# Performance work log

Measured on AMD Instinct MI355X. Metric: run time of the kernel, lower is better.

## Reference

```python
import jax, jax.numpy as jnp
import numpy as np

EPS = 1e-8  # torch F.cosine_similarity eps


def _cosine_logits(emb, mem):
    # emb: [N, C], mem: [S, C] -> [N, S]
    num = emb @ mem.T
    denom = jnp.linalg.norm(emb, axis=1, keepdims=True) * jnp.linalg.norm(mem, axis=1)[None, :]
    return num / jnp.maximum(denom, EPS)


def setup_inputs() -> dict:
    key = jax.random.key(0)
    k1, k2, k3, k4 = jax.random.split(key, 4)
    N, S, C = 8192, 4096, 256
    return {
        "face": jax.random.normal(k1, (N, C), dtype=jnp.float32),
        "speech": jax.random.normal(k2, (N, C), dtype=jnp.float32),
        # init.normal_(mean=0, std=0.5)
        "speech_value_memory": 0.5 * jax.random.normal(k3, (S, C), dtype=jnp.float32),
        "face_key_memory": 0.5 * jax.random.normal(k4, (S, C), dtype=jnp.float32),
    }


def reference(face, speech, speech_value_memory, face_key_memory):
    # speech_encoder runs under torch.no_grad() -> stop_gradient; encoders abstracted as identity.
    speech_emb = jax.lax.stop_gradient(speech)
    face_emb = face

    speech_logits = _cosine_logits(speech_emb, speech_value_memory)      # [N, S]
    speech_address_log = jax.nn.log_softmax(speech_logits, axis=1)
    speech_address = jax.nn.softmax(speech_logits, axis=1)
    speech_emb_recall = speech_address @ speech_value_memory             # [N, C]

    face_logits = _cosine_logits(face_emb, face_key_memory)             # [N, S]
    face_address_log = jax.nn.log_softmax(face_logits, axis=1)
    face_address = jax.nn.softmax(face_logits, axis=1)
    face_emb_recall = face_address @ speech_value_memory                 # [N, C]

    return (speech_emb, speech_emb_recall, face_emb, face_emb_recall,
            speech_address_log, face_address_log)
```

## Files before the change

kernel.cpp:

```cpp
#include <hip/hip_runtime.h>
#include <hip/hip_bf16.h>
#include <cstdint>
#include <cstddef>

typedef __attribute__((ext_vector_type(8))) short bf16x8;
typedef __attribute__((ext_vector_type(4))) float f32x4;

static __device__ __forceinline__ unsigned short f2bf(float f) {
    union { float f; unsigned u; } v; v.f = f;
    return (unsigned short)((v.u + 0x7fffu + ((v.u >> 16) & 1u)) >> 16);
}
static __device__ __forceinline__ float bf2f(unsigned short h) {
    union { unsigned u; float f; } v; v.u = ((unsigned)h) << 16;
    return v.f;
}

static __device__ __forceinline__ void gld_lds16(const unsigned short* g, unsigned short* l) {
    __builtin_amdgcn_global_load_lds(
        (const __attribute__((address_space(1))) void*)g,
        (__attribute__((address_space(3))) void*)l, 16, 0, 0);
}

#define NC 2097152
#define SC 1048576
#define NS 33554432
#define SPLITS 4

__global__ __launch_bounds__(64) void rownorm_kernel(
    const float* __restrict__ face, const float* __restrict__ speech,
    const float* __restrict__ svm, const float* __restrict__ fkm,
    unsigned short* __restrict__ face_n, unsigned short* __restrict__ speech_n,
    unsigned short* __restrict__ svm_n, unsigned short* __restrict__ fkm_n,
    float* __restrict__ out_face, float* __restrict__ out_speech,
    unsigned short* __restrict__ svmT,
    float* __restrict__ out_srecall, float* __restrict__ out_frecall)
{
    const int which = blockIdx.y;
    const int row   = blockIdx.x;
    const int lane  = threadIdx.x;

    if (which == 4) {
        const float4 z = make_float4(0.f, 0.f, 0.f, 0.f);
        *(float4*)(out_srecall + (size_t)row * 256 + lane * 4) = z;
        *(float4*)(out_frecall + (size_t)row * 256 + lane * 4) = z;
        return;
    }
    if (which >= 2 && row >= 4096) return;

    const float* in; unsigned short* nrm; float* cpy = nullptr; bool tr = false;
    if (which == 0)      { in = speech; nrm = speech_n; cpy = out_speech; }
    else if (which == 1) { in = face;   nrm = face_n;   cpy = out_face; }
    else if (which == 2) { in = svm;    nrm = svm_n;    tr = true; }
    else                 { in = fkm;    nrm = fkm_n; }

    const float4 v = *(const float4*)(in + (size_t)row * 256 + lane * 4);
    float ss = v.x * v.x + v.y * v.y + v.z * v.z + v.w * v.w;
    #pragma unroll
    for (int off = 32; off > 0; off >>= 1) ss += __shfl_xor(ss, off);
    const float rn = rsqrtf(ss);

    ushort4 o;
    o.x = f2bf(v.x * rn); o.y = f2bf(v.y * rn);
    o.z = f2bf(v.z * rn); o.w = f2bf(v.w * rn);
    *(ushort4*)(nrm + (size_t)row * 256 + lane * 4) = o;

    if (cpy) *(float4*)(cpy + (size_t)row * 256 + lane * 4) = v;

    if (tr) {
        const int c = lane * 4;
        svmT[(size_t)(c + 0) * 4096 + row] = f2bf(v.x);
        svmT[(size_t)(c + 1) * 4096 + row] = f2bf(v.y);
        svmT[(size_t)(c + 2) * 4096 + row] = f2bf(v.z);
        svmT[(size_t)(c + 3) * 4096 + row] = f2bf(v.w);
    }
}

__global__ __launch_bounds__(256) void gemm_logits_kernel(
    const unsigned short* __restrict__ speech_n,
    const unsigned short* __restrict__ face_n,
    const unsigned short* __restrict__ svm_n,
    const unsigned short* __restrict__ fkm_n,
    unsigned short* __restrict__ logits)
{
    __shared__ unsigned short smem[128 * 32 * 2];
    unsigned short* As = smem;
    unsigned short* Bs = smem + 128 * 32;
    const int side = blockIdx.z;
    const unsigned short* A = side ? face_n : speech_n;
    const unsigned short* B = side ? fkm_n  : svm_n;
    unsigned short* Lg = logits + ((size_t)side * NS);

    const int row0 = blockIdx.y * 128;
    const int col0 = blockIdx.x * 128;
    const int tid  = threadIdx.x;
    const int wave = tid >> 6, lane = tid & 63;
    const int wm = (wave >> 1) * 64, wn = (wave & 1) * 64;
    const int quad = lane >> 4, r16 = lane & 15;

    const int r0 = tid >> 2,          cj0 = tid & 3;
    const int r1 = (tid + 256) >> 2,  cj1 = (tid + 256) & 3;

    f32x4 acc[4][4];
    #pragma unroll
    for (int i = 0; i < 4; i++)
        #pragma unroll
        for (int j = 0; j < 4; j++) acc[i][j] = 0.f;

    for (int k0 = 0; k0 < 256; k0 += 32) {
        gld_lds16(A + (size_t)(row0 + r0) * 256 + k0 + cj0 * 8, As + (size_t)(wave * 64) * 8);
        gld_lds16(B + (size_t)(col0 + r0) * 256 + k0 + cj0 * 8, Bs + (size_t)(wave * 64) * 8);
        gld_lds16(A + (size_t)(row0 + r1) * 256 + k0 + cj1 * 8, As + (size_t)(256 + wave * 64) * 8);
        gld_lds16(B + (size_t)(col0 + r1) * 256 + k0 + cj1 * 8, Bs + (size_t)(256 + wave * 64) * 8);
        __syncthreads();

        bf16x8 af[4], bfr[4];
        #pragma unroll
        for (int i = 0; i < 4; i++) {
            af[i]  = *(const bf16x8*)(&As[(wm + i * 16 + r16) * 32 + quad * 8]);
            bfr[i] = *(const bf16x8*)(&Bs[(wn + i * 16 + r16) * 32 + quad * 8]);
        }
        #pragma unroll
        for (int i = 0; i < 4; i++)
            #pragma unroll
            for (int j = 0; j < 4; j++)
                acc[i][j] = __builtin_amdgcn_mfma_f32_16x16x32_bf16(
                    af[i], bfr[j], acc[i][j], 0, 0, 0);
        __syncthreads();
    }

    unsigned short* tb = smem + wave * 2048;
    #pragma unroll
    for (int h = 0; h < 2; ++h) {
        #pragma unroll
        for (int i2 = 0; i2 < 2; ++i2)
            #pragma unroll
            for (int j = 0; j < 4; ++j)
                #pragma unroll
                for (int rr = 0; rr < 4; ++rr)
                    tb[(i2 * 16 + quad * 4 + rr) * 64 + j * 16 + r16] =
                        f2bf(acc[2 * h + i2][j][rr]);
        __syncthreads();
        #pragma unroll
        for (int p = 0; p < 4; ++p) {
            const int lrow = p * 8 + (lane >> 3);
            const int lcol = (lane & 7) * 8;
            const uint4 v = *(const uint4*)(tb + lrow * 64 + lcol);
            *(uint4*)(Lg + (size_t)(row0 + wm + h * 32 + lrow) * 4096 + col0 + wn + lcol) = v;
        }
        __syncthreads();
    }
}

__global__ __launch_bounds__(256) void softmax_kernel(
    const unsigned short* __restrict__ logits,
    float* __restrict__ lse_ws,
    float* __restrict__ out_slog, float* __restrict__ out_flog)
{
    __shared__ float red[4];
    const int b = blockIdx.x;
    const int side = b >> 13, row = b & 8191;
    const size_t off = (size_t)side * NS + ((size_t)row << 12);
    const unsigned short* lp = logits + off;
    float* op = (side ? out_flog : out_slog) + ((size_t)row << 12);
    const int t = threadIdx.x;

    float x[16];
    float s = 0.f;
    #pragma unroll
    for (int i = 0; i < 2; i++) {
        const int j = t + i * 256;
        unsigned short vv[8];
        *(uint4*)vv = *(const uint4*)(lp + (size_t)j * 8);
        #pragma unroll
        for (int k = 0; k < 8; k++) {
            const float xv = bf2f(vv[k]);
            x[i * 8 + k] = xv;
            s += __expf(xv);
        }
    }
    #pragma unroll
    for (int o = 32; o > 0; o >>= 1) s += __shfl_xor(s, o);
    if ((t & 63) == 0) red[t >> 6] = s;
    __syncthreads();
    s = red[0] + red[1] + red[2] + red[3];
    const float lse = __logf(s);
    if (t == 0) lse_ws[(size_t)side * 8192 + row] = lse;

    #pragma unroll
    for (int i = 0; i < 2; i++) {
        const int j = t + i * 256;
        f32x4 o0, o1;
        o0[0] = x[i*8+0] - lse; o0[1] = x[i*8+1] - lse;
        o0[2] = x[i*8+2] - lse; o0[3] = x[i*8+3] - lse;
        o1[0] = x[i*8+4] - lse; o1[1] = x[i*8+5] - lse;
        o1[2] = x[i*8+6] - lse; o1[3] = x[i*8+7] - lse;
        __builtin_nontemporal_store(o0, (f32x4*)op + j * 2);
        __builtin_nontemporal_store(o1, (f32x4*)op + j * 2 + 1);
    }
}

__global__ __launch_bounds__(256) void gemm_recall_kernel(
    const unsigned short* __restrict__ logits,
    const float* __restrict__ lse,
    const unsigned short* __restrict__ BT,
    float* __restrict__ out_srecall, float* __restrict__ out_frecall)
{
    __shared__ unsigned short As[64 * 32];
    __shared__ unsigned short Bs[256 * 32];
    const int row0  = blockIdx.x * 64;
    const int split = blockIdx.y;
    const int side  = blockIdx.z;
    const unsigned short* A = logits + (size_t)side * NS;
    float* outp = side ? out_frecall : out_srecall;
    const int kbase = split * (4096 / SPLITS);

    const int tid  = threadIdx.x;
    const int wave = tid >> 6, lane = tid & 63;
    const int wn = wave * 64;
    const int quad = lane >> 4, r16 = lane & 15;
    const int arow = tid >> 2, acj = tid & 3;
    const float myl = lse[(size_t)side * 8192 + row0 + arow];

    f32x4 acc[4][4];
    #pragma unroll
    for (int i = 0; i < 4; i++)
        #pragma unroll
        for (int j = 0; j < 4; j++) acc[i][j] = 0.f;

    for (int k0 = kbase; k0 < kbase + 4096 / SPLITS; k0 += 32) {
        unsigned short vv[8];
        *(uint4*)vv = *(const uint4*)(A + (size_t)(row0 + arow) * 4096 + k0 + acj * 8);
        #pragma unroll
        for (int it = 0; it < 4; ++it) {
            const int c = tid + it * 256, r = c >> 2, cj = c & 3;
            gld_lds16(BT + (size_t)r * 4096 + k0 + cj * 8,
                      Bs + (size_t)(it * 256 + wave * 64) * 8);
        }
        unsigned short pv[8];
        #pragma unroll
        for (int k = 0; k < 8; k++) pv[k] = f2bf(__expf(bf2f(vv[k]) - myl));
        *(uint4*)(&As[arow * 32 + acj * 8]) = *(uint4*)pv;
        __syncthreads();

        bf16x8 af[4], bfr[4];
        #pragma unroll
        for (int i = 0; i < 4; i++) {
            af[i]  = *(const bf16x8*)(&As[(i * 16 + r16) * 32 + quad * 8]);
            bfr[i] = *(const bf16x8*)(&Bs[(wn + i * 16 + r16) * 32 + quad * 8]);
        }
        #pragma unroll
        for (int i = 0; i < 4; i++)
            #pragma unroll
            for (int j = 0; j < 4; j++)
                acc[i][j] = __builtin_amdgcn_mfma_f32_16x16x32_bf16(
                    af[i], bfr[j], acc[i][j], 0, 0, 0);
        __syncthreads();
    }

    #pragma unroll
    for (int i = 0; i < 4; i++) {
        #pragma unroll
        for (int j = 0; j < 4; j++) {
            const int r  = row0 + i * 16 + quad * 4;
            const int cc = wn + j * 16 + r16;
            #pragma unroll
            for (int rr = 0; rr < 4; rr++)
                unsafeAtomicAdd(&outp[(size_t)(r + rr) * 256 + cc], acc[i][j][rr]);
        }
    }
}

extern "C" void kernel_launch(void* const* d_in, const int* in_sizes, int n_in,
                              void* d_out, int out_size, void* d_ws, size_t ws_size,
                              hipStream_t stream) {
    const float* face   = (const float*)d_in[0];
    const float* speech = (const float*)d_in[1];
    const float* svm    = (const float*)d_in[2];
    const float* fkm    = (const float*)d_in[3];

    const int N = 8192, S = 4096, C = 256;
    float* out = (float*)d_out;
    float* out_speech  = out;
    float* out_srecall = out + (size_t)N * C;
    float* out_face    = out + 2 * (size_t)N * C;
    float* out_frecall = out + 3 * (size_t)N * C;
    float* out_slog    = out + 4 * (size_t)N * C;
    float* out_flog    = out_slog + (size_t)N * S;

    unsigned short* wsu = (unsigned short*)d_ws;
    unsigned short* speech_n = wsu;
    unsigned short* face_n   = speech_n + NC;
    unsigned short* svm_n    = face_n + NC;
    unsigned short* fkm_n    = svm_n + SC;
    unsigned short* svmT     = fkm_n + SC;
    unsigned short* logits   = svmT + SC;
    float* lse = (float*)(logits + 2 * (size_t)NS);

    dim3 g1(N, 5);
    rownorm_kernel<<<g1, 64, 0, stream>>>(face, speech, svm, fkm,
                                          face_n, speech_n, svm_n, fkm_n,
                                          out_face, out_speech, svmT,
                                          out_srecall, out_frecall);

    dim3 g2(S / 128, N / 128, 2);
    gemm_logits_kernel<<<g2, 256, 0, stream>>>(speech_n, face_n, svm_n, fkm_n, logits);

    softmax_kernel<<<2 * N, 256, 0, stream>>>(logits, lse, out_slog, out_flog);

    dim3 g4(N / 64, SPLITS, 2);
    gemm_recall_kernel<<<g4, 256, 0, stream>>>(logits, lse, svmT,
                                               out_srecall, out_frecall);
}
```

Before: 524.9 us.

## Fuse softmax into logits GEMM epilogue and recall GEMM, dropping softmax pass

Accumulates per-row sum of exponentials via atomics in the logits GEMM epilogue and moves the log-softmax output writes into the recall GEMM, which already reads the logits. This removes a separate softmax kernel and its full re-read of the bf16 logits buffer. It adds atomic traffic and heavier store work in the recall kernel. The sum is taken from fp32 accumulators rather than bf16-rounded logits, a small numeric change.

```diff
diff --git a/kernel.cpp b/kernel.cpp
--- a/kernel.cpp
+++ b/kernel.cpp
@@ -33,7 +33,8 @@
     unsigned short* __restrict__ svm_n, unsigned short* __restrict__ fkm_n,
     float* __restrict__ out_face, float* __restrict__ out_speech,
     unsigned short* __restrict__ svmT,
-    float* __restrict__ out_srecall, float* __restrict__ out_frecall)
+    float* __restrict__ out_srecall, float* __restrict__ out_frecall,
+    float* __restrict__ sumexp)
 {
     const int which = blockIdx.y;
     const int row   = blockIdx.x;
@@ -43,6 +44,7 @@
         const float4 z = make_float4(0.f, 0.f, 0.f, 0.f);
         *(float4*)(out_srecall + (size_t)row * 256 + lane * 4) = z;
         *(float4*)(out_frecall + (size_t)row * 256 + lane * 4) = z;
+        if (lane < 2) sumexp[(size_t)lane * 8192 + row] = 0.f;
         return;
     }
     if (which >= 2 && row >= 4096) return;
@@ -80,7 +82,8 @@
     const unsigned short* __restrict__ face_n,
     const unsigned short* __restrict__ svm_n,
     const unsigned short* __restrict__ fkm_n,
-    unsigned short* __restrict__ logits)
+    unsigned short* __restrict__ logits,
+    float* __restrict__ sumexp)
 {
     __shared__ unsigned short smem[128 * 32 * 2];
     unsigned short* As = smem;
@@ -128,6 +131,20 @@
         __syncthreads();
     }
 
+    #pragma unroll
+    for (int i = 0; i < 4; i++) {
+        #pragma unroll
+        for (int rr = 0; rr < 4; rr++) {
+            float s = 0.f;
+            #pragma unroll
+            for (int j = 0; j < 4; j++) s += __expf(acc[i][j][rr]);
+            #pragma unroll
+            for (int o = 8; o > 0; o >>= 1) s += __shfl_xor(s, o);
+            if (r16 == 0)
+                unsafeAtomicAdd(&sumexp[(size_t)side * 8192 + row0 + wm + i * 16 + quad * 4 + rr], s);
+        }
+    }
+
     unsigned short* tb = smem + wave * 2048;
     #pragma unroll
     for (int h = 0; h < 2; ++h) {
@@ -151,59 +168,12 @@
     }
 }
 
-__global__ __launch_bounds__(256) void softmax_kernel(
-    const unsigned short* __restrict__ logits,
-    float* __restrict__ lse_ws,
-    float* __restrict__ out_slog, float* __restrict__ out_flog)
-{
-    __shared__ float red[4];
-    const int b = blockIdx.x;
-    const int side = b >> 13, row = b & 8191;
-    const size_t off = (size_t)side * NS + ((size_t)row << 12);
-    const unsigned short* lp = logits + off;
-    float* op = (side ? out_flog : out_slog) + ((size_t)row << 12);
-    const int t = threadIdx.x;
-
-    float x[16];
-    float s = 0.f;
-    #pragma unroll
-    for (int i = 0; i < 2; i++) {
-        const int j = t + i * 256;
-        unsigned short vv[8];
-        *(uint4*)vv = *(const uint4*)(lp + (size_t)j * 8);
-        #pragma unroll
-        for (int k = 0; k < 8; k++) {
-            const float xv = bf2f(vv[k]);
-            x[i * 8 + k] = xv;
-            s += __expf(xv);
-        }
-    }
-    #pragma unroll
-    for (int o = 32; o > 0; o >>= 1) s += __shfl_xor(s, o);
-    if ((t & 63) == 0) red[t >> 6] = s;
-    __syncthreads();
-    s = red[0] + red[1] + red[2] + red[3];
-    const float lse = __logf(s);
-    if (t == 0) lse_ws[(size_t)side * 8192 + row] = lse;
-
-    #pragma unroll
-    for (int i = 0; i < 2; i++) {
-        const int j = t + i * 256;
-        f32x4 o0, o1;
-        o0[0] = x[i*8+0] - lse; o0[1] = x[i*8+1] - lse;
-        o0[2] = x[i*8+2] - lse; o0[3] = x[i*8+3] - lse;
-        o1[0] = x[i*8+4] - lse; o1[1] = x[i*8+5] - lse;
-        o1[2] = x[i*8+6] - lse; o1[3] = x[i*8+7] - lse;
-        __builtin_nontemporal_store(o0, (f32x4*)op + j * 2);
-        __builtin_nontemporal_store(o1, (f32x4*)op + j * 2 + 1);
-    }
-}
-
 __global__ __launch_bounds__(256) void gemm_recall_kernel(
     const unsigned short* __restrict__ logits,
-    const float* __restrict__ lse,
+    const float* __restrict__ sumexp,
     const unsigned short* __restrict__ BT,
-    float* __restrict__ out_srecall, float* __restrict__ out_frecall)
+    float* __restrict__ out_srecall, float* __restrict__ out_frecall,
+    float* __restrict__ out_slog, float* __restrict__ out_flog)
 {
     __shared__ unsigned short As[64 * 32];
     __shared__ unsigned short Bs[256 * 32];
@@ -212,6 +182,7 @@
     const int side  = blockIdx.z;
     const unsigned short* A = logits + (size_t)side * NS;
     float* outp = side ? out_frecall : out_srecall;
+    float* slog = side ? out_flog    : out_slog;
     const int kbase = split * (4096 / SPLITS);
 
     const int tid  = threadIdx.x;
@@ -219,7 +190,8 @@
     const int wn = wave * 64;
     const int quad = lane >> 4, r16 = lane & 15;
     const int arow = tid >> 2, acj = tid & 3;
-    const float myl = lse[(size_t)side * 8192 + row0 + arow];
+    const float myl = __logf(sumexp[(size_t)side * 8192 + row0 + arow]);
+    float* slogp = slog + (size_t)(row0 + arow) * 4096 + acj * 8;
 
     f32x4 acc[4][4];
     #pragma unroll
@@ -236,9 +208,17 @@
             gld_lds16(BT + (size_t)r * 4096 + k0 + cj * 8,
                       Bs + (size_t)(it * 256 + wave * 64) * 8);
         }
+        float xs[8];
+        #pragma unroll
+        for (int k = 0; k < 8; k++) xs[k] = bf2f(vv[k]) - myl;
+        f32x4 s0, s1;
+        s0[0] = xs[0]; s0[1] = xs[1]; s0[2] = xs[2]; s0[3] = xs[3];
+        s1[0] = xs[4]; s1[1] = xs[5]; s1[2] = xs[6]; s1[3] = xs[7];
+        __builtin_nontemporal_store(s0, (f32x4*)(slogp + k0));
+        __builtin_nontemporal_store(s1, (f32x4*)(slogp + k0 + 4));
         unsigned short pv[8];
         #pragma unroll
-        for (int k = 0; k < 8; k++) pv[k] = f2bf(__expf(bf2f(vv[k]) - myl));
+        for (int k = 0; k < 8; k++) pv[k] = f2bf(__expf(xs[k]));
         *(uint4*)(&As[arow * 32 + acj * 8]) = *(uint4*)pv;
         __syncthreads();
 
@@ -294,20 +274,20 @@
     unsigned short* fkm_n    = svm_n + SC;
     unsigned short* svmT     = fkm_n + SC;
     unsigned short* logits   = svmT + SC;
-    float* lse = (float*)(logits + 2 * (size_t)NS);
+    float* sumexp = (float*)(logits + 2 * (size_t)NS);
 
     dim3 g1(N, 5);
     rownorm_kernel<<<g1, 64, 0, stream>>>(face, speech, svm, fkm,
                                           face_n, speech_n, svm_n, fkm_n,
                                           out_face, out_speech, svmT,
-                                          out_srecall, out_frecall);
+                                          out_srecall, out_frecall, sumexp);
 
     dim3 g2(S / 128, N / 128, 2);
-    gemm_logits_kernel<<<g2, 256, 0, stream>>>(speech_n, face_n, svm_n, fkm_n, logits);
-
-    softmax_kernel<<<2 * N, 256, 0, stream>>>(logits, lse, out_slog, out_flog);
+    gemm_logits_kernel<<<g2, 256, 0, stream>>>(speech_n, face_n, svm_n, fkm_n,
+                                               logits, sumexp);
 
     dim3 g4(N / 64, SPLITS, 2);
-    gemm_recall_kernel<<<g4, 256, 0, stream>>>(logits, lse, svmT,
-                                               out_srecall, out_frecall);
-}
+    gemm_recall_kernel<<<g4, 256, 0, stream>>>(logits, sumexp, svmT,
+                                               out_srecall, out_frecall,
+                                               out_slog, out_flog);
+}
```

Result: faster. 471.2 us (-10.2%).
